# Performance work log

Hardware: AMD Instinct MI355X
Metric: run time of the kernel (lower is better)

The kernel has to match this reference:

```python
import jax, jax.numpy as jnp
import numpy as np

NUM_CLASSES = 2
THRESH = 0.5          # overlap_thresh
NEGPOS = 3            # neg:pos ratio
VAR0, VAR1 = 0.1, 0.2 # SSD cfg['variance']
B, P, NOBJ = 256, 8732, 32


def setup_inputs() -> dict:
    key = jax.random.key(0)
    k1, k2, k3, k4, k5, k6 = jax.random.split(key, 6)
    loc_data = jax.random.normal(k1, (B, P, 4), jnp.float32)
    conf_data = jax.random.normal(k2, (B, P, NUM_CLASSES), jnp.float32)
    # priors in (cx, cy, w, h) form, normalized coords
    p_cxy = jax.random.uniform(k3, (P, 2), minval=0.0, maxval=1.0)
    p_wh = jax.random.uniform(k4, (P, 2), minval=0.05, maxval=0.4)
    priors = jnp.concatenate([p_cxy, p_wh], axis=1).astype(jnp.float32)
    # ground-truth boxes in (x1, y1, x2, y2) + label, label 0 -> conf target 1
    t_cxy = jax.random.uniform(k5, (B, NOBJ, 2), minval=0.15, maxval=0.85)
    t_wh = jax.random.uniform(k6, (B, NOBJ, 2), minval=0.05, maxval=0.3)
    boxes = jnp.concatenate([t_cxy - t_wh / 2, t_cxy + t_wh / 2], axis=-1)
    labels = jnp.zeros((B, NOBJ, 1), jnp.float32)
    targets = jnp.concatenate([boxes, labels], axis=-1).astype(jnp.float32)
    return {"loc_data": loc_data, "conf_data": conf_data, "priors": priors, "targets": targets}


def _point_form(pr):
    # (cx,cy,w,h) -> (x1,y1,x2,y2)
    return jnp.concatenate([pr[:, :2] - pr[:, 2:] / 2, pr[:, :2] + pr[:, 2:] / 2], axis=1)


def _jaccard(a, b):
    # a: [n,4], b: [m,4] in corner form -> IoU [n,m]
    lt = jnp.maximum(a[:, None, :2], b[None, :, :2])
    rb = jnp.minimum(a[:, None, 2:], b[None, :, 2:])
    wh = jnp.clip(rb - lt, 0.0, None)
    inter = wh[..., 0] * wh[..., 1]
    area_a = ((a[:, 2] - a[:, 0]) * (a[:, 3] - a[:, 1]))[:, None]
    area_b = ((b[:, 2] - b[:, 0]) * (b[:, 3] - b[:, 1]))[None, :]
    return inter / (area_a + area_b - inter)


def _match(truths, labels, priors):
    # truths: [NOBJ,4] corner form, labels: [NOBJ], priors: [P,4] center form
    ov = _jaccard(truths, _point_form(priors))           # [NOBJ, P]
    best_prior_idx = jnp.argmax(ov, axis=1)              # [NOBJ] best prior per truth
    best_truth_overlap = jnp.max(ov, axis=0)             # [P]
    best_truth_idx = jnp.argmax(ov, axis=0)              # [P]
    # ensure each truth keeps its best prior
    best_truth_overlap = best_truth_overlap.at[best_prior_idx].set(2.0)
    best_truth_idx = best_truth_idx.at[best_prior_idx].set(jnp.arange(truths.shape[0]))
    matched = truths[best_truth_idx]                     # [P,4]
    conf = labels[best_truth_idx].astype(jnp.int32) + 1
    conf = jnp.where(best_truth_overlap < THRESH, 0, conf)
    # encode offsets with variances
    g_cxcy = ((matched[:, :2] + matched[:, 2:]) * 0.5 - priors[:, :2]) / (VAR0 * priors[:, 2:])
    g_wh = jnp.log((matched[:, 2:] - matched[:, :2]) / priors[:, 2:]) / VAR1
    return jnp.concatenate([g_cxcy, g_wh], axis=1), conf


def reference(loc_data, conf_data, priors, targets):
    num, nP, C = conf_data.shape
    loc_t, conf_t = jax.vmap(_match, in_axes=(0, 0, None))(
        targets[:, :, :4], targets[:, :, 4], priors)     # [B,P,4], [B,P]
    loc_t = jax.lax.stop_gradient(loc_t)
    pos = conf_t > 0                                     # [B,P]

    # localization: smooth L1 (beta=1), summed over positives
    d = loc_data - loc_t
    ad = jnp.abs(d)
    sl1 = jnp.where(ad < 1.0, 0.5 * d * d, ad - 0.5)
    loss_l = jnp.sum(sl1 * pos[..., None].astype(sl1.dtype))

    # per-prior CE terms: logsumexp - gathered true-class logit
    lse = jax.nn.logsumexp(conf_data, axis=-1)           # [B,P]
    gathered = jnp.take_along_axis(conf_data, conf_t[..., None], axis=-1)[..., 0]
    ce = lse - gathered                                  # [B,P]

    # hard negative mining: rank negatives by ce (positives zeroed)
    loss_c_rank = jnp.where(pos, 0.0, ce)
    loss_idx = jnp.argsort(-loss_c_rank, axis=1)
    idx_rank = jnp.argsort(loss_idx, axis=1)
    num_pos = jnp.sum(pos, axis=1, keepdims=True)        # [B,1] int
    num_neg = jnp.clip(NEGPOS * num_pos, None, nP - 1)
    neg = idx_rank < num_neg

    sel = jnp.logical_or(pos, neg)
    loss_c = jnp.sum(jnp.where(sel, ce, 0.0))

    N = jnp.sum(num_pos).astype(loss_l.dtype)
    return loss_l / N, loss_c / N
```

## Files before the change

### kernel.cpp

```cpp
#include <hip/hip_runtime.h>

#define NP   8732
#define NOBJ 32
#define NB   256
#define NT   1024
#define PPT  9
#define NW   (NT/64)

__device__ __forceinline__ float sl1(float d){
    float ad = fabsf(d);
    return ad < 1.0f ? 0.5f * d * d : ad - 0.5f;
}

__global__ __attribute__((amdgpu_flat_work_group_size(NT, NT),
                          amdgpu_waves_per_eu(4, 4))) void mbox_main(
    const float* __restrict__ loc_data,
    const float* __restrict__ conf_data,
    const float* __restrict__ priors,
    const float* __restrict__ targets,
    float* __restrict__ out_part)
{
    const int b    = blockIdx.x;
    const int tid  = threadIdx.x;
    const int lane = tid & 63;
    const int wid  = tid >> 6;

    __shared__ float s_tx1[NOBJ], s_ty1[NOBJ], s_tx2[NOBJ], s_ty2[NOBJ],
                     s_ta[NOBJ], s_tl[NOBJ];
    __shared__ float s_bto[NP];
    __shared__ unsigned char s_bti[NP];
    __shared__ unsigned long long s_part[NOBJ][NW];
    __shared__ int s_bp[NOBJ];
    __shared__ unsigned long long s_red64[NW];
    __shared__ float s_redf[NW], s_redf2[NW];
    __shared__ int s_redi[NW];

    if (tid < NOBJ){
        const float* tp = targets + ((size_t)b * NOBJ + tid) * 5;
        float x1 = tp[0], y1 = tp[1], x2 = tp[2], y2 = tp[3];
        s_tx1[tid] = x1; s_ty1[tid] = y1; s_tx2[tid] = x2; s_ty2[tid] = y2;
        s_ta[tid]  = (x2 - x1) * (y2 - y1);
        s_tl[tid]  = tp[4];
    }
    __syncthreads();

    float px1[PPT], py1[PPT], px2[PPT], py2[PPT], pa[PPT], bto[PPT];
    int   bti[PPT];
    #pragma unroll
    for (int i = 0; i < PPT; ++i){
        int p = tid + i * NT;
        if (p < NP){
            float4 pr = reinterpret_cast<const float4*>(priors)[p];
            float hx = pr.z * 0.5f, hy = pr.w * 0.5f;
            px1[i] = pr.x - hx; py1[i] = pr.y - hy;
            px2[i] = pr.x + hx; py2[i] = pr.y + hy;
            pa[i]  = (px2[i] - px1[i]) * (py2[i] - py1[i]);
        } else {
            px1[i] = 4e9f; py1[i] = 4e9f; px2[i] = 4e9f; py2[i] = 4e9f;
            pa[i]  = 1.0f;
        }
        bto[i] = -1.0f; bti[i] = 0;
    }

    #pragma unroll 1
    for (int t = 0; t < NOBJ; ++t){
        float tx1 = s_tx1[t], ty1 = s_ty1[t], tx2 = s_tx2[t], ty2 = s_ty2[t];
        float ta  = s_ta[t];
        float bv = -1.0f; int bp = 0;
        #pragma unroll
        for (int i = 0; i < PPT; ++i){
            float lx = fmaxf(tx1, px1[i]);
            float ly = fmaxf(ty1, py1[i]);
            float rx = fminf(tx2, px2[i]);
            float ry = fminf(ty2, py2[i]);
            float w  = fmaxf(rx - lx, 0.0f);
            float h  = fmaxf(ry - ly, 0.0f);
            float inter = w * h;
            float den   = ta + pa[i] - inter;
            float iou   = inter / den;
            if (iou > bto[i]){ bto[i] = iou; bti[i] = t; }
            if (iou > bv){ bv = iou; bp = tid + i * NT; }
        }
        #pragma unroll
        for (int off = 32; off > 0; off >>= 1){
            float ov = __shfl_xor(bv, off);
            int   op = __shfl_xor(bp, off);
            if (ov > bv || (ov == bv && op < bp)){ bv = ov; bp = op; }
        }
        if (lane == 0)
            s_part[t][wid] = ((unsigned long long)__float_as_uint(bv) << 32)
                           | (unsigned)(NP - 1 - bp);
    }

    #pragma unroll
    for (int i = 0; i < PPT; ++i){
        int p = tid + i * NT;
        if (p < NP){
            s_bto[p] = bto[i];
            s_bti[p] = (unsigned char)bti[i];
        }
    }
    __syncthreads();

    if (tid < NOBJ){
        unsigned long long best = 0ull;
        #pragma unroll
        for (int j = 0; j < NW; ++j){
            unsigned long long v = s_part[tid][j];
            if (v > best) best = v;
        }
        s_bp[tid] = NP - 1 - (int)(best & 0xffffffffu);
    }
    __syncthreads();
    if (tid == 0){
        for (int t = 0; t < NOBJ; ++t){
            int p = s_bp[t];
            s_bto[p] = 2.0f;
            s_bti[p] = (unsigned char)t;
        }
    }
    __syncthreads();

    float lossl = 0.0f, sumce = 0.0f;
    int npos = 0;
    float    rnk[PPT];
    unsigned rb_[PPT];
    #pragma unroll
    for (int i = 0; i < PPT; ++i){
        int p = tid + i * NT;
        float rank = 0.0f;
        if (p < NP){
            float ov = s_bto[p];
            int   t  = s_bti[p];
            bool pos = !(ov < 0.5f);
            float2 c = reinterpret_cast<const float2*>(conf_data)[(size_t)b * NP + p];
            float m   = fmaxf(c.x, c.y);
            float lse = m + logf(expf(c.x - m) + expf(c.y - m));
            if (pos){
                int cls = (int)s_tl[t] + 1;
                float g = (cls >= 1) ? c.y : c.x;
                float ce = lse - g;
                ++npos;
                sumce += ce;
                float4 l  = reinterpret_cast<const float4*>(loc_data)[(size_t)b * NP + p];
                float4 pr = reinterpret_cast<const float4*>(priors)[p];
                float mx1 = s_tx1[t], my1 = s_ty1[t], mx2 = s_tx2[t], my2 = s_ty2[t];
                float gcx = ((mx1 + mx2) * 0.5f - pr.x) / (0.1f * pr.z);
                float gcy = ((my1 + my2) * 0.5f - pr.y) / (0.1f * pr.w);
                float gw  = logf((mx2 - mx1) / pr.z) / 0.2f;
                float gh  = logf((my2 - my1) / pr.w) / 0.2f;
                lossl += sl1(l.x - gcx) + sl1(l.y - gcy)
                       + sl1(l.z - gw)  + sl1(l.w - gh);
                rank = 0.0f;
            } else {
                rank = lse - c.x;
            }
        }
        rnk[i] = rank;
        rb_[i] = __float_as_uint(rank);
    }

    #pragma unroll
    for (int off = 32; off > 0; off >>= 1){
        npos  += __shfl_xor(npos,  off);
        sumce += __shfl_xor(sumce, off);
        lossl += __shfl_xor(lossl, off);
    }
    if (lane == 0){ s_redi[wid] = npos; s_redf[wid] = sumce; s_redf2[wid] = lossl; }
    __syncthreads();
    int npos_tot = 0; float sumce_tot = 0.0f, lossl_tot = 0.0f;
    #pragma unroll
    for (int j = 0; j < NW; ++j){
        npos_tot  += s_redi[j];
        sumce_tot += s_redf[j];
        lossl_tot += s_redf2[j];
    }
    __syncthreads();

    int k = 3 * npos_tot; if (k > NP - 1) k = NP - 1;
    unsigned vk = 0u;
    for (int bit = 30; bit >= 0; bit = (bit == 30) ? 28 : bit - 2){
        unsigned c1, c2, c3;
        bool pair = (bit != 30);
        if (pair){
            c1 = vk | (1u << bit); c2 = vk | (2u << bit); c3 = vk | (3u << bit);
        } else {
            c1 = vk | (1u << 30); c2 = 0xffffffffu; c3 = 0xffffffffu;
        }
        unsigned long long pc = 0ull;
        #pragma unroll
        for (int i = 0; i < PPT; ++i){
            unsigned u = rb_[i];
            pc += (u >= c1) ? 1ull : 0ull;
            pc += (u >= c2) ? (1ull << 21) : 0ull;
            pc += (u >= c3) ? (1ull << 42) : 0ull;
        }
        #pragma unroll
        for (int off = 32; off > 0; off >>= 1)
            pc += __shfl_xor(pc, off);
        if (lane == 0) s_red64[wid] = pc;
        __syncthreads();
        unsigned long long tot = 0ull;
        #pragma unroll
        for (int j = 0; j < NW; ++j) tot += s_red64[j];
        __syncthreads();
        int n1 = (int)(tot & 0x1FFFFFull);
        int n2 = (int)((tot >> 21) & 0x1FFFFFull);
        int n3 = (int)((tot >> 42) & 0x1FFFFFull);
        if (pair){
            vk |= (n3 >= k) ? (3u << bit) : (n2 >= k) ? (2u << bit)
                 : (n1 >= k) ? (1u << bit) : 0u;
        } else {
            vk |= (n1 >= k) ? (1u << 30) : 0u;
        }
    }

    int ngt = 0; float sgt = 0.0f;
    #pragma unroll
    for (int i = 0; i < PPT; ++i){
        if (rb_[i] > vk){ ++ngt; sgt += rnk[i]; }
    }
    #pragma unroll
    for (int off = 32; off > 0; off >>= 1){
        ngt += __shfl_xor(ngt, off);
        sgt += __shfl_xor(sgt, off);
    }
    if (lane == 0){ s_redi[wid] = ngt; s_redf[wid] = sgt; }
    __syncthreads();
    int ngt_tot = 0; float sgt_tot = 0.0f;
    #pragma unroll
    for (int j = 0; j < NW; ++j){ ngt_tot += s_redi[j]; sgt_tot += s_redf[j]; }

    if (tid == 0){
        float lossc = sumce_tot;
        if (k > 0)
            lossc += sgt_tot + (float)(k - ngt_tot) * __uint_as_float(vk);
        out_part[b * 4 + 0] = lossl_tot;
        out_part[b * 4 + 1] = lossc;
        out_part[b * 4 + 2] = (float)npos_tot;
    }
}

__global__ void mbox_final(const float* __restrict__ part, float* __restrict__ out){
    int tid = threadIdx.x;
    int lane = tid & 63, wid = tid >> 6;
    float ll = part[tid * 4 + 0];
    float lc = part[tid * 4 + 1];
    float np_ = part[tid * 4 + 2];
    #pragma unroll
    for (int off = 32; off > 0; off >>= 1){
        ll  += __shfl_xor(ll,  off);
        lc  += __shfl_xor(lc,  off);
        np_ += __shfl_xor(np_, off);
    }
    __shared__ float sl[4], sc[4], sn[4];
    if (lane == 0){ sl[wid] = ll; sc[wid] = lc; sn[wid] = np_; }
    __syncthreads();
    if (tid == 0){
        float L = sl[0] + sl[1] + sl[2] + sl[3];
        float C = sc[0] + sc[1] + sc[2] + sc[3];
        float N = sn[0] + sn[1] + sn[2] + sn[3];
        out[0] = L / N;
        out[1] = C / N;
    }
}

extern "C" void kernel_launch(void* const* d_in, const int* in_sizes, int n_in,
                              void* d_out, int out_size, void* d_ws, size_t ws_size,
                              hipStream_t stream){
    const float* loc     = (const float*)d_in[0];
    const float* conf    = (const float*)d_in[1];
    const float* priors  = (const float*)d_in[2];
    const float* targets = (const float*)d_in[3];
    float* part = (float*)d_ws;
    float* out  = (float*)d_out;
    mbox_main<<<NB, NT, 0, stream>>>(loc, conf, priors, targets, part);
    mbox_final<<<1, NB, 0, stream>>>(part, out);
}
```

Baseline: 192.5 us.

## Split IoU matching into per-prior and per-truth passes to cut registers and syncs

The IoU matching is now two separate passes. In the first, each thread takes one prior at a time and loops over all truths, writing that prior's best truth straight to shared memory. In the second, each wave finds the best prior for two truths using wave shuffles, which removes the shared partial-result array, its cross-wave reduction and one barrier. The rank array is also dropped and rebuilt from its bit pattern, to save registers. The cost is that every IoU, including its divide, is now computed twice, and priors are reloaded from global memory in the second pass.

After: 228.5 us. +18.7%, slower.

```diff
diff --git a/kernel.cpp b/kernel.cpp
--- a/kernel.cpp
+++ b/kernel.cpp
@@ -6,6 +6,7 @@
 #define NT   1024
 #define PPT  9
 #define NW   (NT/64)
+#define KA2  137
 
 __device__ __forceinline__ float sl1(float d){
     float ad = fabsf(d);
@@ -29,7 +30,6 @@
                      s_ta[NOBJ], s_tl[NOBJ];
     __shared__ float s_bto[NP];
     __shared__ unsigned char s_bti[NP];
-    __shared__ unsigned long long s_part[NOBJ][NW];
     __shared__ int s_bp[NOBJ];
     __shared__ unsigned long long s_red64[NW];
     __shared__ float s_redf[NW], s_redf2[NW];
@@ -44,74 +44,87 @@
     }
     __syncthreads();
 
-    float px1[PPT], py1[PPT], px2[PPT], py2[PPT], pa[PPT], bto[PPT];
-    int   bti[PPT];
-    #pragma unroll
+    #pragma unroll 1
     for (int i = 0; i < PPT; ++i){
         int p = tid + i * NT;
         if (p < NP){
             float4 pr = reinterpret_cast<const float4*>(priors)[p];
-            float hx = pr.z * 0.5f, hy = pr.w * 0.5f;
-            px1[i] = pr.x - hx; py1[i] = pr.y - hy;
-            px2[i] = pr.x + hx; py2[i] = pr.y + hy;
-            pa[i]  = (px2[i] - px1[i]) * (py2[i] - py1[i]);
-        } else {
-            px1[i] = 4e9f; py1[i] = 4e9f; px2[i] = 4e9f; py2[i] = 4e9f;
-            pa[i]  = 1.0f;
-        }
-        bto[i] = -1.0f; bti[i] = 0;
-    }
-
-    #pragma unroll 1
-    for (int t = 0; t < NOBJ; ++t){
-        float tx1 = s_tx1[t], ty1 = s_ty1[t], tx2 = s_tx2[t], ty2 = s_ty2[t];
-        float ta  = s_ta[t];
-        float bv = -1.0f; int bp = 0;
-        #pragma unroll
-        for (int i = 0; i < PPT; ++i){
-            float lx = fmaxf(tx1, px1[i]);
-            float ly = fmaxf(ty1, py1[i]);
-            float rx = fminf(tx2, px2[i]);
-            float ry = fminf(ty2, py2[i]);
-            float w  = fmaxf(rx - lx, 0.0f);
-            float h  = fmaxf(ry - ly, 0.0f);
-            float inter = w * h;
-            float den   = ta + pa[i] - inter;
-            float iou   = inter / den;
-            if (iou > bto[i]){ bto[i] = iou; bti[i] = t; }
-            if (iou > bv){ bv = iou; bp = tid + i * NT; }
-        }
+            float hx  = pr.z * 0.5f, hy = pr.w * 0.5f;
+            float px1 = pr.x - hx, py1 = pr.y - hy;
+            float px2 = pr.x + hx, py2 = pr.y + hy;
+            float pa  = (px2 - px1) * (py2 - py1);
+            float bto = -1.0f; int bti = 0;
+            #pragma unroll 4
+            for (int t = 0; t < NOBJ; ++t){
+                float lx = fmaxf(s_tx1[t], px1);
+                float ly = fmaxf(s_ty1[t], py1);
+                float rx = fminf(s_tx2[t], px2);
+                float ry = fminf(s_ty2[t], py2);
+                float w  = fmaxf(rx - lx, 0.0f);
+                float h  = fmaxf(ry - ly, 0.0f);
+                float inter = w * h;
+                float den   = s_ta[t] + pa - inter;
+                float iou   = inter / den;
+                if (iou > bto){ bto = iou; bti = t; }
+            }
+            s_bto[p] = bto;
+            s_bti[p] = (unsigned char)bti;
+        }
+    }
+
+    {
+        const int t0 = 2 * wid, t1 = 2 * wid + 1;
+        float atx1 = s_tx1[t0], aty1 = s_ty1[t0], atx2 = s_tx2[t0],
+              aty2 = s_ty2[t0], ata = s_ta[t0];
+        float btx1 = s_tx1[t1], bty1 = s_ty1[t1], btx2 = s_tx2[t1],
+              bty2 = s_ty2[t1], bta = s_ta[t1];
+        float bv0 = -1.0f, bv1 = -1.0f;
+        int   bp0 = 0,     bp1 = 0;
+        #pragma unroll 2
+        for (int k = 0; k < KA2; ++k){
+            int p = lane + (k << 6);
+            if (p < NP){
+                float4 pr = reinterpret_cast<const float4*>(priors)[p];
+                float hx  = pr.z * 0.5f, hy = pr.w * 0.5f;
+                float px1 = pr.x - hx, py1 = pr.y - hy;
+                float px2 = pr.x + hx, py2 = pr.y + hy;
+                float pa  = (px2 - px1) * (py2 - py1);
+                {
+                    float lx = fmaxf(atx1, px1), ly = fmaxf(aty1, py1);
+                    float rx = fminf(atx2, px2), ry = fminf(aty2, py2);
+                    float w  = fmaxf(rx - lx, 0.0f), h = fmaxf(ry - ly, 0.0f);
+                    float inter = w * h;
+                    float iou = inter / (ata + pa - inter);
+                    if (iou > bv0){ bv0 = iou; bp0 = p; }
+                }
+                {
+                    float lx = fmaxf(btx1, px1), ly = fmaxf(bty1, py1);
+                    float rx = fminf(btx2, px2), ry = fminf(bty2, py2);
+                    float w  = fmaxf(rx - lx, 0.0f), h = fmaxf(ry - ly, 0.0f);
+                    float inter = w * h;
+                    float iou = inter / (bta + pa - inter);
+                    if (iou > bv1){ bv1 = iou; bp1 = p; }
+                }
+            }
+        }
+        unsigned long long k0 = ((unsigned long long)__float_as_uint(bv0) << 32)
+                              | (unsigned)(NP - 1 - bp0);
+        unsigned long long k1 = ((unsigned long long)__float_as_uint(bv1) << 32)
+                              | (unsigned)(NP - 1 - bp1);
         #pragma unroll
         for (int off = 32; off > 0; off >>= 1){
-            float ov = __shfl_xor(bv, off);
-            int   op = __shfl_xor(bp, off);
-            if (ov > bv || (ov == bv && op < bp)){ bv = ov; bp = op; }
-        }
-        if (lane == 0)
-            s_part[t][wid] = ((unsigned long long)__float_as_uint(bv) << 32)
-                           | (unsigned)(NP - 1 - bp);
-    }
-
-    #pragma unroll
-    for (int i = 0; i < PPT; ++i){
-        int p = tid + i * NT;
-        if (p < NP){
-            s_bto[p] = bto[i];
-            s_bti[p] = (unsigned char)bti[i];
-        }
-    }
-    __syncthreads();
-
-    if (tid < NOBJ){
-        unsigned long long best = 0ull;
-        #pragma unroll
-        for (int j = 0; j < NW; ++j){
-            unsigned long long v = s_part[tid][j];
-            if (v > best) best = v;
-        }
-        s_bp[tid] = NP - 1 - (int)(best & 0xffffffffu);
-    }
-    __syncthreads();
+            unsigned long long o0 = __shfl_xor(k0, off);
+            unsigned long long o1 = __shfl_xor(k1, off);
+            if (o0 > k0) k0 = o0;
+            if (o1 > k1) k1 = o1;
+        }
+        if (lane == 0){
+            s_bp[t0] = NP - 1 - (int)(k0 & 0xffffffffu);
+            s_bp[t1] = NP - 1 - (int)(k1 & 0xffffffffu);
+        }
+    }
+    __syncthreads();
+
     if (tid == 0){
         for (int t = 0; t < NOBJ; ++t){
             int p = s_bp[t];
@@ -123,7 +136,6 @@
 
     float lossl = 0.0f, sumce = 0.0f;
     int npos = 0;
-    float    rnk[PPT];
     unsigned rb_[PPT];
     #pragma unroll
     for (int i = 0; i < PPT; ++i){
@@ -156,7 +168,6 @@
                 rank = lse - c.x;
             }
         }
-        rnk[i] = rank;
         rb_[i] = __float_as_uint(rank);
     }
 
@@ -218,7 +229,7 @@
     int ngt = 0; float sgt = 0.0f;
     #pragma unroll
     for (int i = 0; i < PPT; ++i){
-        if (rb_[i] > vk){ ++ngt; sgt += rnk[i]; }
+        if (rb_[i] > vk){ ++ngt; sgt += __uint_as_float(rb_[i]); }
     }
     #pragma unroll
     for (int off = 32; off > 0; off >>= 1){
```
